# Performance work log

Hardware: AMD Instinct MI355X
Metric: run time of the kernel (lower is better)

## Reference

```python
import jax, jax.numpy as jnp
import numpy as np

C, G, S, L, B = 16, 8192, 8, 3, 32


def setup_inputs() -> dict:
    key = jax.random.key(0)
    kx, kI = jax.random.split(key)
    # x: valuation vector over G ground atoms per batch element, in [0,1)
    x = jax.random.uniform(kx, (B, G), dtype=jnp.float32)
    # I: precomputed index tensor [C, G, S, L], indices into the G axis of x
    I = jax.random.randint(kI, (C, G, S, L), 0, G, dtype=jnp.int64)
    return {"x": x, "I": I}


def reference(x, I):
    # Equivalent of: for each clause i, gather(V_tild, 1, I_i) -> prod over L -> sum over S
    # torch gather semantics: out[b, g, s, l] = x[b, I[i, g, s, l]]
    # Vectorized over all clauses at once; no repeat/broadcast materialization beyond the gather.
    gathered = x[:, I]                        # [B, C, G, S, L]
    body = jnp.prod(gathered, axis=-1)        # conjunction over L body literals -> [B, C, G, S]
    clause_val = jnp.sum(body, axis=-1)       # sum over S substitutions -> [B, C, G]
    # torch.stack over clauses puts C first: [C, B, G]
    return jnp.transpose(clause_val, (1, 0, 2))
```

## Files before the change

kernel.cpp:

```cpp
#include <hip/hip_runtime.h>
#include <hip/hip_fp16.h>
#include <stdint.h>

#define Cc 16
#define Gg 8192
#define Ss 8
#define Ll 3
#define Bb 32

#define ZS 4
#define THREADS 512
#define ITERS 2

__global__ __launch_bounds__(256) void build_xh(const float* __restrict__ x,
                                                uint4* __restrict__ xh) {
    int t = blockIdx.x * 256 + threadIdx.x;
    int z = t >> 13;
    int g = t & (Gg - 1);
    uint32_t d[4];
    #pragma unroll
    for (int j = 0; j < 4; ++j) {
        __half2 h = __floats2half2_rn(x[(size_t)(8 * z + 2 * j) * Gg + g],
                                      x[(size_t)(8 * z + 2 * j + 1) * Gg + g]);
        d[j] = *(const uint32_t*)&h;
    }
    uint32_t s = (g >> 3) & 1u;
    xh[t] = s ? make_uint4(d[2], d[3], d[0], d[1])
              : make_uint4(d[0], d[1], d[2], d[3]);
}

__device__ __forceinline__ void clause_eval(const uint2* __restrict__ xl2,
                                            const int4 q[6], float acc[8]) {
    int idx[Ss * Ll] = {q[0].x, q[0].y, q[0].z, q[0].w, q[1].x, q[1].y, q[1].z, q[1].w,
                        q[2].x, q[2].y, q[2].z, q[2].w, q[3].x, q[3].y, q[3].z, q[3].w,
                        q[4].x, q[4].y, q[4].z, q[4].w, q[5].x, q[5].y, q[5].z, q[5].w};
    uint2 r0[Ss * Ll], r1[Ss * Ll];
    #pragma unroll
    for (int k = 0; k < Ss * Ll; ++k) {
        uint32_t u = (uint32_t)idx[k];
        uint32_t a0 = (u << 1) | ((u >> 3) & 1u);
        r0[k] = xl2[a0];
        r1[k] = xl2[a0 ^ 1u];
    }
    #pragma unroll
    for (int s = 0; s < Ss; ++s) {
        const int k0 = 3 * s, k1 = 3 * s + 1, k2 = 3 * s + 2;
        const uint32_t pa[4] = {r0[k0].x, r0[k0].y, r1[k0].x, r1[k0].y};
        const uint32_t pb[4] = {r0[k1].x, r0[k1].y, r1[k1].x, r1[k1].y};
        const uint32_t pd[4] = {r0[k2].x, r0[k2].y, r1[k2].x, r1[k2].y};
        #pragma unroll
        for (int j = 0; j < 4; ++j) {
            __half2 a = *(const __half2*)&pa[j];
            __half2 b = *(const __half2*)&pb[j];
            __half2 d = *(const __half2*)&pd[j];
            __half2 p = __hmul2(__hmul2(a, b), d);
            float2 pf = __half22float2(p);
            acc[2 * j] += pf.x;
            acc[2 * j + 1] += pf.y;
        }
    }
}

__global__ __launch_bounds__(THREADS) void clause_f16(const uint4* __restrict__ xh,
                                                      const int* __restrict__ I,
                                                      float* __restrict__ out) {
    __shared__ uint4 xl[Gg];
    const int tid = threadIdx.x;
    const int z = blockIdx.y;
    const int c = blockIdx.x >> 3;
    const int gbase = (blockIdx.x & 7) * (THREADS * ITERS);

    {
        const uint4* gs = xh + (size_t)z * Gg;
        uint4 t0[8];
        #pragma unroll
        for (int i = 0; i < 8; ++i) t0[i] = gs[tid + i * THREADS];
        #pragma unroll
        for (int i = 0; i < 8; ++i) xl[tid + i * THREADS] = t0[i];
        uint4 t1[8];
        #pragma unroll
        for (int i = 0; i < 8; ++i) t1[i] = gs[tid + (8 + i) * THREADS];
        #pragma unroll
        for (int i = 0; i < 8; ++i) xl[tid + (8 + i) * THREADS] = t1[i];
    }

    const int g0 = gbase + tid;
    const int g1 = gbase + THREADS + tid;
    const int4* ip0 = (const int4*)(I + ((size_t)c * Gg + g0) * (Ss * Ll));
    const int4* ip1 = (const int4*)(I + ((size_t)c * Gg + g1) * (Ss * Ll));
    int4 q0[6], q1[6];
    #pragma unroll
    for (int k = 0; k < 6; ++k) q0[k] = ip0[k];
    #pragma unroll
    for (int k = 0; k < 6; ++k) q1[k] = ip1[k];

    __syncthreads();

    const uint2* xl2 = (const uint2*)xl;
    float* opb = out + ((size_t)(c * Bb + 8 * z)) * Gg;

    {
        float acc[8] = {0, 0, 0, 0, 0, 0, 0, 0};
        clause_eval(xl2, q0, acc);
        #pragma unroll
        for (int j = 0; j < 8; ++j)
            opb[(size_t)j * Gg + g0] = acc[j];
    }
    {
        float acc[8] = {0, 0, 0, 0, 0, 0, 0, 0};
        clause_eval(xl2, q1, acc);
        #pragma unroll
        for (int j = 0; j < 8; ++j)
            opb[(size_t)j * Gg + g1] = acc[j];
    }
}

__global__ __launch_bounds__(256) void clause_kernel_direct(const float* __restrict__ x,
                                                            const int* __restrict__ I,
                                                            float* __restrict__ out) {
    const int tid = threadIdx.x;
    const int b = tid & 31;
    const int j = tid >> 5;
    const int g = blockIdx.x * 8 + j;
    const int c = blockIdx.y;

    const int* Icg = I + (size_t)(c * Gg + g) * (Ss * Ll);
    float sum = 0.f;
    #pragma unroll
    for (int s = 0; s < Ss; ++s) {
        float p0 = x[(size_t)b * Gg + Icg[3 * s + 0]];
        float p1 = x[(size_t)b * Gg + Icg[3 * s + 1]];
        float p2 = x[(size_t)b * Gg + Icg[3 * s + 2]];
        sum += p0 * p1 * p2;
    }
    out[(size_t)(c * Bb + b) * Gg + g] = sum;
}

extern "C" void kernel_launch(void* const* d_in, const int* in_sizes, int n_in,
                              void* d_out, int out_size, void* d_ws, size_t ws_size,
                              hipStream_t stream) {
    const float* x = (const float*)d_in[0];
    const int* I = (const int*)d_in[1];
    float* out = (float*)d_out;

    const size_t xh_bytes = (size_t)ZS * Gg * sizeof(uint4);

    if (ws_size >= xh_bytes) {
        uint4* xh = (uint4*)d_ws;
        build_xh<<<(ZS * Gg) / 256, 256, 0, stream>>>(x, xh);
        clause_f16<<<dim3((Cc * Gg) / (THREADS * ITERS), ZS), THREADS, 0, stream>>>(xh, I, out);
    } else {
        clause_kernel_direct<<<dim3(Gg / 8, Cc), 256, 0, stream>>>(x, I, out);
    }
}
```

Before: 81.64 us.

## Split clause work between LDS gathers and global gathers from a g-major table

Adds a second fp16 table laid out g-major, holding all 32 batch values per ground atom in 64 contiguous bytes. Half of the ground atoms are processed with the existing LDS-resident table. The other half use four threads per atom that gather 16-byte chunks straight from global memory, which moves load off the LDS. The LDS gathers are also widened to 16 bytes and double-buffered, and the bank-swizzle is removed. The cost is an extra table build and write, plus redundant I reads for the global-path atoms (each index row is read by four threads), and LDS bank conflicts may change because the swizzle is gone.

```diff
diff --git a/kernel.cpp b/kernel.cpp
--- a/kernel.cpp
+++ b/kernel.cpp
@@ -7,13 +7,12 @@
 #define Ss 8
 #define Ll 3
 #define Bb 32
-
 #define ZS 4
 #define THREADS 512
-#define ITERS 2
 
-__global__ __launch_bounds__(256) void build_xh(const float* __restrict__ x,
-                                                uint4* __restrict__ xh) {
+__global__ __launch_bounds__(256) void build_tables(const float* __restrict__ x,
+                                                    uint4* __restrict__ xh,
+                                                    uint4* __restrict__ xw) {
     int t = blockIdx.x * 256 + threadIdx.x;
     int z = t >> 13;
     int g = t & (Gg - 1);
@@ -24,51 +23,41 @@
                                       x[(size_t)(8 * z + 2 * j + 1) * Gg + g]);
         d[j] = *(const uint32_t*)&h;
     }
-    uint32_t s = (g >> 3) & 1u;
-    xh[t] = s ? make_uint4(d[2], d[3], d[0], d[1])
-              : make_uint4(d[0], d[1], d[2], d[3]);
+    uint4 o = make_uint4(d[0], d[1], d[2], d[3]);
+    xh[t] = o;
+    xw[(size_t)g * 4 + z] = o;
 }
 
-__device__ __forceinline__ void clause_eval(const uint2* __restrict__ xl2,
-                                            const int4 q[6], float acc[8]) {
-    int idx[Ss * Ll] = {q[0].x, q[0].y, q[0].z, q[0].w, q[1].x, q[1].y, q[1].z, q[1].w,
-                        q[2].x, q[2].y, q[2].z, q[2].w, q[3].x, q[3].y, q[3].z, q[3].w,
-                        q[4].x, q[4].y, q[4].z, q[4].w, q[5].x, q[5].y, q[5].z, q[5].w};
-    uint2 r0[Ss * Ll], r1[Ss * Ll];
+__device__ __forceinline__ void flat24(const int4 q[6], int idx[24]) {
     #pragma unroll
-    for (int k = 0; k < Ss * Ll; ++k) {
-        uint32_t u = (uint32_t)idx[k];
-        uint32_t a0 = (u << 1) | ((u >> 3) & 1u);
-        r0[k] = xl2[a0];
-        r1[k] = xl2[a0 ^ 1u];
-    }
-    #pragma unroll
-    for (int s = 0; s < Ss; ++s) {
-        const int k0 = 3 * s, k1 = 3 * s + 1, k2 = 3 * s + 2;
-        const uint32_t pa[4] = {r0[k0].x, r0[k0].y, r1[k0].x, r1[k0].y};
-        const uint32_t pb[4] = {r0[k1].x, r0[k1].y, r1[k1].x, r1[k1].y};
-        const uint32_t pd[4] = {r0[k2].x, r0[k2].y, r1[k2].x, r1[k2].y};
-        #pragma unroll
-        for (int j = 0; j < 4; ++j) {
-            __half2 a = *(const __half2*)&pa[j];
-            __half2 b = *(const __half2*)&pb[j];
-            __half2 d = *(const __half2*)&pd[j];
-            __half2 p = __hmul2(__hmul2(a, b), d);
-            float2 pf = __half22float2(p);
-            acc[2 * j] += pf.x;
-            acc[2 * j + 1] += pf.y;
-        }
+    for (int k = 0; k < 6; ++k) {
+        idx[4 * k + 0] = q[k].x; idx[4 * k + 1] = q[k].y;
+        idx[4 * k + 2] = q[k].z; idx[4 * k + 3] = q[k].w;
     }
 }
 
-__global__ __launch_bounds__(THREADS) void clause_f16(const uint4* __restrict__ xh,
-                                                      const int* __restrict__ I,
-                                                      float* __restrict__ out) {
+__device__ __forceinline__ void acc_oct(const uint4& a4, const uint4& b4,
+                                        const uint4& d4, float acc[8]) {
+    const __half2* a = (const __half2*)&a4;
+    const __half2* b = (const __half2*)&b4;
+    const __half2* d = (const __half2*)&d4;
+    #pragma unroll
+    for (int j = 0; j < 4; ++j) {
+        __half2 p = __hmul2(__hmul2(a[j], b[j]), d[j]);
+        float2 pf = __half22float2(p);
+        acc[2 * j]     += pf.x;
+        acc[2 * j + 1] += pf.y;
+    }
+}
+
+__global__ __launch_bounds__(THREADS) void clause_hybrid(const uint4* __restrict__ xh,
+                                                         const uint4* __restrict__ xw,
+                                                         const int* __restrict__ I,
+                                                         float* __restrict__ out) {
     __shared__ uint4 xl[Gg];
     const int tid = threadIdx.x;
+    const int bx = blockIdx.x;
     const int z = blockIdx.y;
-    const int c = blockIdx.x >> 3;
-    const int gbase = (blockIdx.x & 7) * (THREADS * ITERS);
 
     {
         const uint4* gs = xh + (size_t)z * Gg;
@@ -77,41 +66,73 @@
         for (int i = 0; i < 8; ++i) t0[i] = gs[tid + i * THREADS];
         #pragma unroll
         for (int i = 0; i < 8; ++i) xl[tid + i * THREADS] = t0[i];
-        uint4 t1[8];
         #pragma unroll
-        for (int i = 0; i < 8; ++i) t1[i] = gs[tid + (8 + i) * THREADS];
+        for (int i = 0; i < 8; ++i) t0[i] = gs[tid + (8 + i) * THREADS];
         #pragma unroll
-        for (int i = 0; i < 8; ++i) xl[tid + (8 + i) * THREADS] = t1[i];
+        for (int i = 0; i < 8; ++i) xl[tid + (8 + i) * THREADS] = t0[i];
     }
 
-    const int g0 = gbase + tid;
-    const int g1 = gbase + THREADS + tid;
-    const int4* ip0 = (const int4*)(I + ((size_t)c * Gg + g0) * (Ss * Ll));
-    const int4* ip1 = (const int4*)(I + ((size_t)c * Gg + g1) * (Ss * Ll));
-    int4 q0[6], q1[6];
+    const int cd = bx >> 3;
+    const int gd = (bx & 7) * 512 + tid;
+    const int4* ipd = (const int4*)(I + ((size_t)cd * Gg + gd) * (Ss * Ll));
+    int4 qd[6];
     #pragma unroll
-    for (int k = 0; k < 6; ++k) q0[k] = ip0[k];
+    for (int k = 0; k < 6; ++k) qd[k] = ipd[k];
+
+    const int chunk = z * 128 + bx;
+    const int ct = chunk >> 5;
+    const int eid = tid >> 2;
+    const int sub = tid & 3;
+    const int gt = 4096 + (chunk & 31) * 128 + eid;
+    const int4* ipt = (const int4*)(I + ((size_t)ct * Gg + gt) * (Ss * Ll));
+    int4 qt[6];
     #pragma unroll
-    for (int k = 0; k < 6; ++k) q1[k] = ip1[k];
+    for (int k = 0; k < 6; ++k) qt[k] = ipt[k];
 
     __syncthreads();
 
-    const uint2* xl2 = (const uint2*)xl;
-    float* opb = out + ((size_t)(c * Bb + 8 * z)) * Gg;
+    int idxt[24];
+    flat24(qt, idxt);
+    uint4 vt[24];
+    #pragma unroll
+    for (int k = 0; k < 24; ++k)
+        vt[k] = xw[(size_t)idxt[k] * 4 + sub];
+
+    int idxd[24];
+    flat24(qd, idxd);
+    float accd[8] = {0, 0, 0, 0, 0, 0, 0, 0};
+    {
+        uint4 vd[2][6];
+        #pragma unroll
+        for (int m = 0; m < 6; ++m) vd[0][m] = xl[idxd[m]];
+        #pragma unroll
+        for (int r = 0; r < 4; ++r) {
+            if (r < 3) {
+                #pragma unroll
+                for (int m = 0; m < 6; ++m) vd[(r + 1) & 1][m] = xl[idxd[6 * (r + 1) + m]];
+            }
+            const uint4* cvd = vd[r & 1];
+            acc_oct(cvd[0], cvd[1], cvd[2], accd);
+            acc_oct(cvd[3], cvd[4], cvd[5], accd);
+        }
+    }
 
     {
-        float acc[8] = {0, 0, 0, 0, 0, 0, 0, 0};
-        clause_eval(xl2, q0, acc);
+        float* opd = out + ((size_t)(cd * Bb + 8 * z)) * Gg + gd;
         #pragma unroll
         for (int j = 0; j < 8; ++j)
-            opb[(size_t)j * Gg + g0] = acc[j];
+            opd[(size_t)j * Gg] = accd[j];
     }
+
     {
-        float acc[8] = {0, 0, 0, 0, 0, 0, 0, 0};
-        clause_eval(xl2, q1, acc);
+        float acct[8] = {0, 0, 0, 0, 0, 0, 0, 0};
+        #pragma unroll
+        for (int s = 0; s < Ss; ++s)
+            acc_oct(vt[3 * s], vt[3 * s + 1], vt[3 * s + 2], acct);
+        float* opt = out + ((size_t)(ct * Bb + 8 * sub)) * Gg + gt;
         #pragma unroll
         for (int j = 0; j < 8; ++j)
-            opb[(size_t)j * Gg + g1] = acc[j];
+            opt[(size_t)j * Gg] = acct[j];
     }
 }
 
@@ -143,12 +164,13 @@
     const int* I = (const int*)d_in[1];
     float* out = (float*)d_out;
 
-    const size_t xh_bytes = (size_t)ZS * Gg * sizeof(uint4);
+    const size_t tbl_bytes = (size_t)ZS * Gg * sizeof(uint4);
 
-    if (ws_size >= xh_bytes) {
+    if (ws_size >= 2 * tbl_bytes) {
         uint4* xh = (uint4*)d_ws;
-        build_xh<<<(ZS * Gg) / 256, 256, 0, stream>>>(x, xh);
-        clause_f16<<<dim3((Cc * Gg) / (THREADS * ITERS), ZS), THREADS, 0, stream>>>(xh, I, out);
+        uint4* xw = (uint4*)((char*)d_ws + tbl_bytes);
+        build_tables<<<(ZS * Gg) / 256, 256, 0, stream>>>(x, xh, xw);
+        clause_hybrid<<<dim3(128, ZS), THREADS, 0, stream>>>(xh, xw, I, out);
     } else {
         clause_kernel_direct<<<dim3(Gg / 8, Cc), 256, 0, stream>>>(x, I, out);
     }
```

Result: no change. 82.19 us (+0.7%).
